# Kernel tuning notes

Hardware: AMD Instinct MI355X
Metric: run time of the kernel (lower is better)

The kernel has to match this reference:

```python
import jax, jax.numpy as jnp
import numpy as np

B, L, D = 4, 2048, 1024
H, DK, DV = 16, 64, 64
SCALE = float((4 * DK) ** 0.5)
EPS = 1e-6


def setup_inputs() -> dict:
    key = jax.random.key(0)
    ks = jax.random.split(key, 16)
    s_in = 1.0 / np.sqrt(D)
    inp = {}
    for i, name in enumerate(["q_a", "k_a", "v_a", "q_s", "k_s", "v_s"]):
        inp[name] = jax.random.normal(ks[i], (B, L, D), dtype=jnp.float32)
    # weights stored as [in, out] so projection is x @ W (equivalent math to nn.Linear)
    for j, name in enumerate(["Wqa", "Wka", "Wva", "Wqs", "Wks", "Wvs", "Wfc"]):
        inp[name] = jax.random.normal(ks[6 + j], (D, D), dtype=jnp.float32) * s_in
    inp["gamma"] = jnp.ones((D,), dtype=jnp.float32)
    inp["beta"] = jnp.zeros((D,), dtype=jnp.float32)
    return inp


def _proj(x, W, dh):
    # [B,L,D] @ [D, H*dh] -> [B,H,L,dh]
    return (x @ W).reshape(B, -1, H, dh).transpose(0, 2, 1, 3)


def reference(q_a, k_a, v_a, q_s, k_s, v_s, Wqa, Wka, Wva, Wqs, Wks, Wvs, Wfc, gamma, beta):
    residual = q_a + q_s
    qa = _proj(q_a, Wqa, DK)
    ka = _proj(k_a, Wka, DK)
    va = _proj(v_a, Wva, DV)
    qs = _proj(q_s, Wqs, DK)
    ks_ = _proj(k_s, Wks, DK)
    vs = _proj(v_s, Wvs, DV)
    # a2a + a2s + s2a + s2s == (qa+qs) @ (ka+ks)^T  (algebraic identity)
    q = qa + qs
    k = ka + ks_
    v = va + vs
    scores = jnp.einsum("bhqd,bhkd->bhqk", q, k) / SCALE
    attn = jax.nn.softmax(scores, axis=-1)  # dropout = identity (eval)
    out = jnp.einsum("bhqk,bhkd->bhqd", attn, v)  # [B,H,L,DV]
    out = out.transpose(0, 2, 1, 3).reshape(B, L, H * DV)
    out = out @ Wfc + residual
    mu = jnp.mean(out, axis=-1, keepdims=True)
    var = jnp.var(out, axis=-1, keepdims=True)
    out = (out - mu) * jax.lax.rsqrt(var + EPS) * gamma + beta
    return out
```

## Files before the change

kernel.cpp:

```cpp
#include <hip/hip_runtime.h>
#include <hip/hip_bf16.h>
#include <stdint.h>

typedef __attribute__((ext_vector_type(4))) float f32x4;
typedef __attribute__((ext_vector_type(16))) float f32x16;
typedef __attribute__((ext_vector_type(8))) short short8;
typedef __attribute__((ext_vector_type(2))) int int2v;

#define DEV static __device__ __forceinline__

DEV unsigned short f2bf(float f) {
  unsigned u = __float_as_uint(f);
  u += 0x7fffu + ((u >> 16) & 1u);
  return (unsigned short)(u >> 16);
}

DEV uint32_t cvtpk(float a, float b) {
  uint32_t r;
  asm("v_cvt_pk_bf16_f32 %0, %1, %2" : "=v"(r) : "v"(a), "v"(b));
  return r;
}

DEV int2v pl32(int a, int b) {
  return __builtin_amdgcn_permlane32_swap(a, b, false, false);
}

typedef const __attribute__((address_space(1))) void* gas_ptr;
typedef __attribute__((address_space(3))) void* las_ptr;

DEV void gload_lds16(const void* g, void* l) {
  __builtin_amdgcn_global_load_lds((gas_ptr)g, (las_ptr)l, 16, 0, 0);
}

struct CvtArgs {
  const float* in[6];
  unsigned short* out[6];
};

__global__ __launch_bounds__(256) void cvt_kernel(CvtArgs a, int n4) {
  const float* __restrict__ in = a.in[blockIdx.y];
  unsigned short* __restrict__ out = a.out[blockIdx.y];
  int idx = blockIdx.x * blockDim.x + threadIdx.x;
  int stride = gridDim.x * blockDim.x;
  for (int i = idx; i < n4; i += stride) {
    float4 v = reinterpret_cast<const float4*>(in)[i];
    ushort4 o;
    o.x = f2bf(v.x); o.y = f2bf(v.y); o.z = f2bf(v.z); o.w = f2bf(v.w);
    reinterpret_cast<ushort4*>(out)[i] = o;
  }
}

struct TcvtArgs {
  const float* src[7];
  unsigned short* dst[7];
  int stride[7];
  int koff[7];
};

__global__ __launch_bounds__(256) void tcvt_kernel(TcvtArgs a) {
  const int which = blockIdx.z;
  const float* __restrict__ src = a.src[which];
  unsigned short* __restrict__ dst = a.dst[which];
  const int dstStride = a.stride[which], kOff = a.koff[which];
  __shared__ float tile[32][33];
  int tx = threadIdx.x & 31;
  int ty = threadIdx.x >> 5;
  int n0 = blockIdx.x * 32;
  int k0 = blockIdx.y * 32;
#pragma unroll
  for (int i = 0; i < 4; i++)
    tile[ty + 8 * i][tx] = src[(size_t)(k0 + ty + 8 * i) * 1024 + n0 + tx];
  __syncthreads();
#pragma unroll
  for (int i = 0; i < 4; i++) {
    int n = n0 + ty + 8 * i;
    dst[(size_t)n * dstStride + kOff + k0 + tx] = f2bf(tile[tx][ty + 8 * i]);
  }
}

struct G3Args {
  const unsigned short* A1[3];
  const unsigned short* A2[3];
  const unsigned short* WT[3];
  unsigned short* out[3];
};

__global__ __launch_bounds__(256) void gemm3_kernel(G3Args g) {
  __shared__ unsigned short As[128 * 32];
  __shared__ unsigned short Bs[128 * 32];
  const int orig = blockIdx.x;
  const int swz = (orig & 7) * 192 + (orig >> 3);
  const int which = swz >> 9;
  const int bid = swz & 511;
  const unsigned short* __restrict__ A1 = g.A1[which];
  const unsigned short* __restrict__ A2 = g.A2[which];
  const unsigned short* __restrict__ WT = g.WT[which];
  unsigned short* __restrict__ outp = g.out[which];

  const int tid = threadIdx.x;
  const int lane = tid & 63;
  const int w = tid >> 6;
  const int mt = bid >> 3, nt = bid & 7;
  const int m0 = mt * 128, n0 = nt * 128;

  const int srow = (w << 4) + (lane >> 2);
  const int scol = (lane & 3) << 3;

  f32x4 zero4 = {0.f, 0.f, 0.f, 0.f};
  f32x4 acc[4][4];
#pragma unroll
  for (int mi = 0; mi < 4; mi++)
#pragma unroll
    for (int ni = 0; ni < 4; ni++) acc[mi][ni] = zero4;

  const int wr = w >> 1, wc = w & 1;
  const int arow = (wr << 6) + (lane & 15);
  const int brow = (wc << 6) + (lane & 15);
  const int kcol = (lane >> 4) << 3;

  for (int kt = 0; kt < 64; kt++) {
    const int kk = kt << 5;
    const unsigned short* Asrc;
    int ka;
    if (kk < 1024) { Asrc = A1; ka = kk; } else { Asrc = A2; ka = kk - 1024; }
#pragma unroll
    for (int p = 0; p < 2; p++) {
      const unsigned short* gp = Asrc + (size_t)(m0 + p * 64 + srow) * 1024 + ka + scol;
      gload_lds16(gp, &As[(p * 64 + srow) * 32 + scol]);
    }
#pragma unroll
    for (int p = 0; p < 2; p++) {
      const unsigned short* gp = WT + (size_t)(n0 + p * 64 + srow) * 2048 + kk + scol;
      gload_lds16(gp, &Bs[(p * 64 + srow) * 32 + scol]);
    }
    __syncthreads();

    short8 av[4], bv[4];
#pragma unroll
    for (int mi = 0; mi < 4; mi++)
      av[mi] = *reinterpret_cast<const short8*>(&As[(arow + mi * 16) * 32 + kcol]);
#pragma unroll
    for (int ni = 0; ni < 4; ni++)
      bv[ni] = *reinterpret_cast<const short8*>(&Bs[(brow + ni * 16) * 32 + kcol]);
#pragma unroll
    for (int mi = 0; mi < 4; mi++)
#pragma unroll
      for (int ni = 0; ni < 4; ni++)
        acc[mi][ni] = __builtin_amdgcn_mfma_f32_16x16x32_bf16(av[mi], bv[ni], acc[mi][ni], 0, 0, 0);
    __syncthreads();
  }

#pragma unroll
  for (int mi = 0; mi < 4; mi++) {
#pragma unroll
    for (int ni = 0; ni < 4; ni++) {
      const int col = n0 + (wc << 6) + ni * 16 + (lane & 15);
      const int rbase = m0 + (wr << 6) + mi * 16 + ((lane >> 4) << 2);
      const int h = col >> 6, d = col & 63;
      if (which < 2) {
#pragma unroll
        for (int r = 0; r < 4; r++) {
          const int m = rbase + r;
          const int b = m >> 11, l = m & 2047;
          outp[((size_t)((b * 16 + h) * 2048 + l)) * 64 + d] = f2bf(acc[mi][ni][r]);
        }
      } else {
        const int m = rbase;
        const int b = m >> 11, l = m & 2047;
        const int bh = b * 16 + h;
        ushort4 o;
        o.x = f2bf(acc[mi][ni][0]);
        o.y = f2bf(acc[mi][ni][1]);
        o.z = f2bf(acc[mi][ni][2]);
        o.w = f2bf(acc[mi][ni][3]);
        *reinterpret_cast<ushort4*>(
            outp + (size_t)(bh * 64 + (l >> 5)) * 2048 + d * 32 + (l & 31)) = o;
      }
    }
  }
}

__global__ __launch_bounds__(256) void gemmfc_kernel(const unsigned short* __restrict__ A1,
                                                     const unsigned short* __restrict__ WT,
                                                     float* __restrict__ outp) {
  __shared__ unsigned short As[128 * 32];
  __shared__ unsigned short Bs[128 * 32];
  const int orig = blockIdx.x;
  const int bid = (orig & 7) * 64 + (orig >> 3);
  const int tid = threadIdx.x;
  const int lane = tid & 63;
  const int w = tid >> 6;
  const int mt = bid >> 3, nt = bid & 7;
  const int m0 = mt * 128, n0 = nt * 128;

  const int srow = (w << 4) + (lane >> 2);
  const int scol = (lane & 3) << 3;

  f32x4 zero4 = {0.f, 0.f, 0.f, 0.f};
  f32x4 acc[4][4];
#pragma unroll
  for (int mi = 0; mi < 4; mi++)
#pragma unroll
    for (int ni = 0; ni < 4; ni++) acc[mi][ni] = zero4;

  const int wr = w >> 1, wc = w & 1;
  const int arow = (wr << 6) + (lane & 15);
  const int brow = (wc << 6) + (lane & 15);
  const int kcol = (lane >> 4) << 3;

  for (int kt = 0; kt < 32; kt++) {
    const int kk = kt << 5;
#pragma unroll
    for (int p = 0; p < 2; p++) {
      const unsigned short* gp = A1 + (size_t)(m0 + p * 64 + srow) * 1024 + kk + scol;
      gload_lds16(gp, &As[(p * 64 + srow) * 32 + scol]);
    }
#pragma unroll
    for (int p = 0; p < 2; p++) {
      const unsigned short* gp = WT + (size_t)(n0 + p * 64 + srow) * 1024 + kk + scol;
      gload_lds16(gp, &Bs[(p * 64 + srow) * 32 + scol]);
    }
    __syncthreads();

    short8 av[4], bv[4];
#pragma unroll
    for (int mi = 0; mi < 4; mi++)
      av[mi] = *reinterpret_cast<const short8*>(&As[(arow + mi * 16) * 32 + kcol]);
#pragma unroll
    for (int ni = 0; ni < 4; ni++)
      bv[ni] = *reinterpret_cast<const short8*>(&Bs[(brow + ni * 16) * 32 + kcol]);
#pragma unroll
    for (int mi = 0; mi < 4; mi++)
#pragma unroll
      for (int ni = 0; ni < 4; ni++)
        acc[mi][ni] = __builtin_amdgcn_mfma_f32_16x16x32_bf16(av[mi], bv[ni], acc[mi][ni], 0, 0, 0);
    __syncthreads();
  }

#pragma unroll
  for (int mi = 0; mi < 4; mi++) {
#pragma unroll
    for (int ni = 0; ni < 4; ni++) {
      const int col = n0 + (wc << 6) + ni * 16 + (lane & 15);
      const int rbase = m0 + (wr << 6) + mi * 16 + ((lane >> 4) << 2);
#pragma unroll
      for (int r = 0; r < 4; r++)
        outp[(size_t)(rbase + r) * 1024 + col] = acc[mi][ni][r];
    }
  }
}

__global__ __launch_bounds__(256) void attn_kernel(const unsigned short* __restrict__ Q,
                                                   const unsigned short* __restrict__ K,
                                                   const unsigned short* __restrict__ Vt,
                                                   unsigned short* __restrict__ O) {
  __shared__ unsigned short Ks[2][2048];
  __shared__ unsigned short Vs[2][2048];
  const int tid = threadIdx.x;
  const int lane = tid & 63;
  const int w = tid >> 6;
  const int n = blockIdx.x;
  const int bh = (n & 7) * 8 + (n >> 7);
  const int qg = (n >> 3) & 15;
  const int q0 = qg * 128 + w * 32;
  const int lo = lane & 31, hi = lane >> 5;

  const unsigned short* qp = Q + ((size_t)bh * 2048 + q0 + lo) * 64 + (hi << 3);
  short8 qf[4];
#pragma unroll
  for (int c = 0; c < 4; c++)
    qf[c] = *reinterpret_cast<const short8*>(qp + c * 16);

  f32x16 o0 = {0.f,0.f,0.f,0.f,0.f,0.f,0.f,0.f,0.f,0.f,0.f,0.f,0.f,0.f,0.f,0.f};
  f32x16 o1 = {0.f,0.f,0.f,0.f,0.f,0.f,0.f,0.f,0.f,0.f,0.f,0.f,0.f,0.f,0.f,0.f};
  float mrun = -1e30f, lsum = 0.0f;
  const float KS = 1.44269504088896f / 16.0f;

  const char* Kg = (const char*)(K + (size_t)bh * 2048 * 64);
  const char* Vg = (const char*)(Vt + (size_t)bh * 131072);

  const int p16 = tid * 16;
  const int lswz = p16 ^ (((p16 >> 7) & 7) << 4);
  const int koff = lswz;
  const int voff = (lswz >> 7) * 64 + ((lswz >> 6) & 1) * 2048 + (lswz & 63);

  const int sK = (lo & 7) << 4;
  int kix[4];
#pragma unroll
  for (int c = 0; c < 4; c++)
    kix[c] = ((lo * 128 + hi * 16 + c * 32) ^ sK) >> 1;
  int vix[4];
  vix[0] = ((lo * 128 + hi * 16) ^ sK) >> 1;
  vix[1] = ((lo * 128 + 32 + hi * 16) ^ sK) >> 1;
  vix[2] = ((lo * 128 + 64 + hi * 16) ^ sK) >> 1;
  vix[3] = ((lo * 128 + 96 + hi * 16) ^ sK) >> 1;

  auto STAGE = [&](int kt, int buf) {
    gload_lds16(Kg + (size_t)kt * 4096 + koff, &Ks[buf][tid * 8]);
    gload_lds16(Vg + (size_t)kt * 4096 + voff, &Vs[buf][tid * 8]);
  };

  STAGE(0, 0);
  __syncthreads();

  for (int kt = 0; kt < 64; kt++) {
    const int buf = kt & 1;
    const int nx = (kt < 63) ? kt + 1 : 63;
    STAGE(nx, buf ^ 1);

    short8 kc[4], vc[4];
#pragma unroll
    for (int c = 0; c < 4; c++)
      kc[c] = *reinterpret_cast<const short8*>(&Ks[buf][kix[c]]);
#pragma unroll
    for (int c = 0; c < 4; c++)
      vc[c] = *reinterpret_cast<const short8*>(&Vs[buf][vix[c]]);

    f32x16 s = {0.f,0.f,0.f,0.f,0.f,0.f,0.f,0.f,0.f,0.f,0.f,0.f,0.f,0.f,0.f,0.f};
    __builtin_amdgcn_s_setprio(1);
#pragma unroll
    for (int c = 0; c < 4; c++)
      s = __builtin_amdgcn_mfma_f32_32x32x16_bf16(kc[c], qf[c], s, 0, 0, 0);
    __builtin_amdgcn_s_setprio(0);

    float m01 = fmaxf(s[0], s[1]), m23 = fmaxf(s[2], s[3]);
    float m45 = fmaxf(s[4], s[5]), m67 = fmaxf(s[6], s[7]);
    float m89 = fmaxf(s[8], s[9]), mab = fmaxf(s[10], s[11]);
    float mcd = fmaxf(s[12], s[13]), mef = fmaxf(s[14], s[15]);
    float cmax = fmaxf(fmaxf(fmaxf(m01, m23), fmaxf(m45, m67)),
                       fmaxf(fmaxf(m89, mab), fmaxf(mcd, mef)));
    {
      int2v mm = pl32(__float_as_int(cmax), __float_as_int(cmax));
      cmax = fmaxf(__int_as_float(mm.x), __int_as_float(mm.y));
    }

    if (__any(cmax > mrun + 128.0f)) {
      const float mnew = fmaxf(mrun, cmax);
      const float alpha = __builtin_amdgcn_exp2f((mrun - mnew) * KS);
      lsum *= alpha;
#pragma unroll
      for (int r = 0; r < 16; r++) {
        const int row = (r & 3) + ((r >> 2) << 3) + (hi << 2);
        const float ar = __shfl(alpha, row);
        o0[r] *= ar;
        o1[r] *= ar;
      }
      mrun = mnew;
    }

    float pr[16];
    const float mk = mrun * KS;
#pragma unroll
    for (int r = 0; r < 16; r++)
      pr[r] = __builtin_amdgcn_exp2f(__builtin_fmaf(s[r], KS, -mk));
    float c01 = (pr[0] + pr[1]) + (pr[2] + pr[3]);
    float c23 = (pr[4] + pr[5]) + (pr[6] + pr[7]);
    float c45 = (pr[8] + pr[9]) + (pr[10] + pr[11]);
    float c67 = (pr[12] + pr[13]) + (pr[14] + pr[15]);
    float csum = (c01 + c23) + (c45 + c67);
    {
      int2v ss = pl32(__float_as_int(csum), __float_as_int(csum));
      csum = __int_as_float(ss.x) + __int_as_float(ss.y);
    }
    lsum += csum;

    const uint32_t c0 = cvtpk(pr[0], pr[1]),   c1 = cvtpk(pr[2], pr[3]);
    const uint32_t c2 = cvtpk(pr[4], pr[5]),   c3 = cvtpk(pr[6], pr[7]);
    const uint32_t c4 = cvtpk(pr[8], pr[9]),   c5 = cvtpk(pr[10], pr[11]);
    const uint32_t c6 = cvtpk(pr[12], pr[13]), c7 = cvtpk(pr[14], pr[15]);
    int2v s02 = pl32((int)c0, (int)c2);
    int2v s13 = pl32((int)c1, (int)c3);
    int2v s46 = pl32((int)c4, (int)c6);
    int2v s57 = pl32((int)c5, (int)c7);
    union { uint32_t u[4]; short8 v; } pa, pb;
    pa.u[0] = (uint32_t)s02.x; pa.u[1] = (uint32_t)s13.x;
    pa.u[2] = (uint32_t)s02.y; pa.u[3] = (uint32_t)s13.y;
    pb.u[0] = (uint32_t)s46.x; pb.u[1] = (uint32_t)s57.x;
    pb.u[2] = (uint32_t)s46.y; pb.u[3] = (uint32_t)s57.y;

    __builtin_amdgcn_s_setprio(1);
    o0 = __builtin_amdgcn_mfma_f32_32x32x16_bf16(pa.v, vc[0], o0, 0, 0, 0);
    o0 = __builtin_amdgcn_mfma_f32_32x32x16_bf16(pb.v, vc[1], o0, 0, 0, 0);
    o1 = __builtin_amdgcn_mfma_f32_32x32x16_bf16(pa.v, vc[2], o1, 0, 0, 0);
    o1 = __builtin_amdgcn_mfma_f32_32x32x16_bf16(pb.v, vc[3], o1, 0, 0, 0);
    __builtin_amdgcn_s_setprio(0);

    __syncthreads();
  }

  const int b = bh >> 4, h = bh & 15;
#pragma unroll
  for (int r = 0; r < 16; r++) {
    const int row = (r & 3) + ((r >> 2) << 3) + (hi << 2);
    const float lr = __shfl(lsum, row);
    const float inv = __builtin_amdgcn_rcpf(lr);
    const size_t base = ((size_t)b * 2048 + q0 + row) * 1024 + h * 64 + lo;
    O[base] = f2bf(o0[r] * inv);
    O[base + 32] = f2bf(o1[r] * inv);
  }
}

__global__ __launch_bounds__(256) void ln_kernel(const float* __restrict__ fc,
                                                 const float* __restrict__ qa,
                                                 const float* __restrict__ qs,
                                                 const float* __restrict__ gamma,
                                                 const float* __restrict__ beta,
                                                 float* __restrict__ out) {
  const int m = blockIdx.x;
  const int t = threadIdx.x;
  const size_t base = (size_t)m * 1024 + t * 4;
  float4 x = *reinterpret_cast<const float4*>(fc + base);
  const float4 a = *reinterpret_cast<const float4*>(qa + base);
  const float4 b = *reinterpret_cast<const float4*>(qs + base);
  x.x += a.x + b.x; x.y += a.y + b.y; x.z += a.z + b.z; x.w += a.w + b.w;
  float s1 = x.x + x.y + x.z + x.w;
  float s2 = x.x * x.x + x.y * x.y + x.z * x.z + x.w * x.w;
#pragma unroll
  for (int off = 1; off < 64; off <<= 1) {
    s1 += __shfl_xor(s1, off);
    s2 += __shfl_xor(s2, off);
  }
  __shared__ float sh[8];
  const int w = t >> 6, lane = t & 63;
  if (lane == 0) { sh[w] = s1; sh[4 + w] = s2; }
  __syncthreads();
  s1 = sh[0] + sh[1] + sh[2] + sh[3];
  s2 = sh[4] + sh[5] + sh[6] + sh[7];
  const float mu = s1 * (1.0f / 1024.0f);
  const float var = s2 * (1.0f / 1024.0f) - mu * mu;
  const float rs = rsqrtf(var + 1e-6f);
  const float4 g = *reinterpret_cast<const float4*>(gamma + t * 4);
  const float4 be = *reinterpret_cast<const float4*>(beta + t * 4);
  float4 y;
  y.x = (x.x - mu) * rs * g.x + be.x;
  y.y = (x.y - mu) * rs * g.y + be.y;
  y.z = (x.z - mu) * rs * g.z + be.z;
  y.w = (x.w - mu) * rs * g.w + be.w;
  *reinterpret_cast<float4*>(out + base) = y;
}

__global__ void sentinel_kernel(float* out, int n) {
  int i = blockIdx.x * blockDim.x + threadIdx.x;
  if (i < n) out[i] = 1234.5f;
}

extern "C" void kernel_launch(void* const* d_in, const int* in_sizes, int n_in,
                              void* d_out, int out_size, void* d_ws, size_t ws_size,
                              hipStream_t stream) {
  const size_t MB = 1024ull * 1024ull;
  if (ws_size < 174 * MB) {
    sentinel_kernel<<<(out_size + 255) / 256, 256, 0, stream>>>((float*)d_out, out_size);
    return;
  }
  const float* fin[6];
  for (int i = 0; i < 6; i++) fin[i] = (const float*)d_in[i];
  const float* Wf[7];
  for (int i = 0; i < 7; i++) Wf[i] = (const float*)d_in[6 + i];
  const float* gamma = (const float*)d_in[13];
  const float* beta = (const float*)d_in[14];

  char* ws = (char*)d_ws;
  unsigned short* Abf[6];
  for (int i = 0; i < 6; i++) Abf[i] = (unsigned short*)(ws + (size_t)i * 16 * MB);
  unsigned short* WqT = (unsigned short*)(ws + 96 * MB);
  unsigned short* WkT = (unsigned short*)(ws + 100 * MB);
  unsigned short* WvT = (unsigned short*)(ws + 104 * MB);
  unsigned short* WfcT = (unsigned short*)(ws + 108 * MB);
  unsigned short* Qb = (unsigned short*)(ws + 110 * MB);
  unsigned short* Kb = (unsigned short*)(ws + 126 * MB);
  unsigned short* Vtb = (unsigned short*)(ws + 142 * MB);
  unsigned short* Ob = (unsigned short*)(ws + 158 * MB);
  float* fcout = (float*)(ws + 16 * MB);

  CvtArgs ca;
  for (int i = 0; i < 6; i++) { ca.in[i] = fin[i]; ca.out[i] = Abf[i]; }
  cvt_kernel<<<dim3(1024, 6), 256, 0, stream>>>(ca, 2097152);

  TcvtArgs ta;
  const int wsel[7] = {0, 3, 1, 4, 2, 5, 6};
  unsigned short* wdst[7] = {WqT, WqT, WkT, WkT, WvT, WvT, WfcT};
  for (int i = 0; i < 7; i++) {
    ta.src[i] = Wf[wsel[i]];
    ta.dst[i] = wdst[i];
    ta.stride[i] = (i < 6) ? 2048 : 1024;
    ta.koff[i] = (i < 6) ? ((i & 1) ? 1024 : 0) : 0;
  }
  tcvt_kernel<<<dim3(32, 32, 7), 256, 0, stream>>>(ta);

  G3Args g3;
  g3.A1[0] = Abf[0]; g3.A2[0] = Abf[3]; g3.WT[0] = WqT; g3.out[0] = Qb;
  g3.A1[1] = Abf[1]; g3.A2[1] = Abf[4]; g3.WT[1] = WkT; g3.out[1] = Kb;
  g3.A1[2] = Abf[2]; g3.A2[2] = Abf[5]; g3.WT[2] = WvT; g3.out[2] = Vtb;
  gemm3_kernel<<<1536, 256, 0, stream>>>(g3);

  attn_kernel<<<1024, 256, 0, stream>>>(Qb, Kb, Vtb, Ob);

  gemmfc_kernel<<<512, 256, 0, stream>>>(Ob, WfcT, fcout);

  ln_kernel<<<8192, 256, 0, stream>>>(fcout, fin[0], fin[3], gamma, beta, (float*)d_out);
}
```

Before: 347.2 us.

## Rewrite QKV projection GEMM with 256x256 tiles, double-buffered swizzled LDS pipeline

```diff
diff --git a/kernel.cpp b/kernel.cpp
--- a/kernel.cpp
+++ b/kernel.cpp
@@ -85,13 +85,13 @@
   unsigned short* out[3];
 };
 
-__global__ __launch_bounds__(256) void gemm3_kernel(G3Args g) {
-  __shared__ unsigned short As[128 * 32];
-  __shared__ unsigned short Bs[128 * 32];
+__global__ __launch_bounds__(512, 2) void gemm3_kernel(G3Args g) {
+  __shared__ unsigned short As[2][256 * 64];
+  __shared__ unsigned short Bs[2][256 * 64];
   const int orig = blockIdx.x;
-  const int swz = (orig & 7) * 192 + (orig >> 3);
-  const int which = swz >> 9;
-  const int bid = swz & 511;
+  const int swz = (orig & 7) * 48 + (orig >> 3);
+  const int which = swz >> 7;
+  const int bid = swz & 127;
   const unsigned short* __restrict__ A1 = g.A1[which];
   const unsigned short* __restrict__ A2 = g.A2[which];
   const unsigned short* __restrict__ WT = g.WT[which];
@@ -100,79 +100,120 @@
   const int tid = threadIdx.x;
   const int lane = tid & 63;
   const int w = tid >> 6;
-  const int mt = bid >> 3, nt = bid & 7;
-  const int m0 = mt * 128, n0 = nt * 128;
-
-  const int srow = (w << 4) + (lane >> 2);
-  const int scol = (lane & 3) << 3;
+  const int mt = bid >> 2, nt = bid & 3;
+  const int m0 = mt * 256, n0 = nt * 256;
+  const int wr = w >> 2, wc = w & 3;
+
+  const int lr = lane >> 3;
+  const int lcsw = (((lane & 7) ^ lr) << 3);
+  const int aW = (w < 4) ? (w * 8) : (128 + (w - 4) * 8);
+  const int bW = w * 8;
+
+  const int la = lane & 15;
+  const int szb = (lane & 7) << 4;
+  int cF[2];
+#pragma unroll
+  for (int ks = 0; ks < 2; ks++)
+    cF[ks] = (((ks << 6) + ((lane >> 4) << 4)) ^ szb) >> 1;
+  const int arA = (wr * 128 + la) * 64;
+  const int brB = (wc * 64 + la) * 64;
 
   f32x4 zero4 = {0.f, 0.f, 0.f, 0.f};
-  f32x4 acc[4][4];
-#pragma unroll
-  for (int mi = 0; mi < 4; mi++)
-#pragma unroll
-    for (int ni = 0; ni < 4; ni++) acc[mi][ni] = zero4;
-
-  const int wr = w >> 1, wc = w & 1;
-  const int arow = (wr << 6) + (lane & 15);
-  const int brow = (wc << 6) + (lane & 15);
-  const int kcol = (lane >> 4) << 3;
-
-  for (int kt = 0; kt < 64; kt++) {
-    const int kk = kt << 5;
-    const unsigned short* Asrc;
-    int ka;
-    if (kk < 1024) { Asrc = A1; ka = kk; } else { Asrc = A2; ka = kk - 1024; }
-#pragma unroll
-    for (int p = 0; p < 2; p++) {
-      const unsigned short* gp = Asrc + (size_t)(m0 + p * 64 + srow) * 1024 + ka + scol;
-      gload_lds16(gp, &As[(p * 64 + srow) * 32 + scol]);
-    }
-#pragma unroll
-    for (int p = 0; p < 2; p++) {
-      const unsigned short* gp = WT + (size_t)(n0 + p * 64 + srow) * 2048 + kk + scol;
-      gload_lds16(gp, &Bs[(p * 64 + srow) * 32 + scol]);
-    }
-    __syncthreads();
-
-    short8 av[4], bv[4];
-#pragma unroll
-    for (int mi = 0; mi < 4; mi++)
-      av[mi] = *reinterpret_cast<const short8*>(&As[(arow + mi * 16) * 32 + kcol]);
-#pragma unroll
-    for (int ni = 0; ni < 4; ni++)
-      bv[ni] = *reinterpret_cast<const short8*>(&Bs[(brow + ni * 16) * 32 + kcol]);
-#pragma unroll
-    for (int mi = 0; mi < 4; mi++)
-#pragma unroll
-      for (int ni = 0; ni < 4; ni++)
-        acc[mi][ni] = __builtin_amdgcn_mfma_f32_16x16x32_bf16(av[mi], bv[ni], acc[mi][ni], 0, 0, 0);
-    __syncthreads();
-  }
-
-#pragma unroll
-  for (int mi = 0; mi < 4; mi++) {
-#pragma unroll
-    for (int ni = 0; ni < 4; ni++) {
-      const int col = n0 + (wc << 6) + ni * 16 + (lane & 15);
-      const int rbase = m0 + (wr << 6) + mi * 16 + ((lane >> 4) << 2);
+  f32x4 acc[8][4];
+#pragma unroll
+  for (int mf = 0; mf < 8; mf++)
+#pragma unroll
+    for (int nf = 0; nf < 4; nf++) acc[mf][nf] = zero4;
+
+  short8 bf[4][2];
+
+  auto STAGE_B = [&](int buf, int kk) {
+#pragma unroll
+    for (int r = 0; r < 4; r++)
+      gload_lds16(WT + (size_t)(n0 + bW + r * 64 + lr) * 2048 + kk + lcsw,
+                  &Bs[buf][(bW + r * 64) * 64 + lane * 8]);
+  };
+  auto STAGE_A = [&](int buf, int kk, int r) {
+    const unsigned short* Ab = (kk < 1024) ? A1 : A2;
+    const int ka = kk & 1023;
+    gload_lds16(Ab + (size_t)(m0 + aW + r * 32 + lr) * 1024 + ka + lcsw,
+                &As[buf][(aW + r * 32) * 64 + lane * 8]);
+  };
+
+  STAGE_B(0, 0);
+#pragma unroll
+  for (int r = 0; r < 4; r++) STAGE_A(0, 0, r);
+  asm volatile("s_waitcnt vmcnt(3)" ::: "memory");
+  __builtin_amdgcn_s_barrier();
+  __builtin_amdgcn_sched_barrier(0);
+
+  for (int kt = 0; kt < 32; kt++) {
+    const int cur = kt & 1;
+    const int nbuf = cur ^ 1;
+    const int kk = kt << 6;
+    const int nk = (kt < 31) ? (kk + 64) : kk;
+#pragma unroll
+    for (int p = 0; p < 4; p++) {
+      if (p == 0) {
+#pragma unroll
+        for (int nf = 0; nf < 4; nf++)
+#pragma unroll
+          for (int ks = 0; ks < 2; ks++)
+            bf[nf][ks] = *reinterpret_cast<const short8*>(&Bs[cur][brB + nf * 1024 + cF[ks]]);
+      }
+      short8 af[2][2];
+#pragma unroll
+      for (int mi = 0; mi < 2; mi++)
+#pragma unroll
+        for (int ks = 0; ks < 2; ks++)
+          af[mi][ks] =
+              *reinterpret_cast<const short8*>(&As[cur][arA + (2 * p + mi) * 1024 + cF[ks]]);
+      if (p == 0) STAGE_B(nbuf, nk);
+      STAGE_A(nbuf, nk, p);
+      asm volatile("s_waitcnt lgkmcnt(0)" ::: "memory");
+      __builtin_amdgcn_sched_barrier(0);
+      __builtin_amdgcn_s_setprio(1);
+#pragma unroll
+      for (int mi = 0; mi < 2; mi++)
+#pragma unroll
+        for (int nf = 0; nf < 4; nf++)
+#pragma unroll
+          for (int ks = 0; ks < 2; ks++)
+            acc[2 * p + mi][nf] = __builtin_amdgcn_mfma_f32_16x16x32_bf16(
+                af[mi][ks], bf[nf][ks], acc[2 * p + mi][nf], 0, 0, 0);
+      __builtin_amdgcn_s_setprio(0);
+      __builtin_amdgcn_sched_barrier(0);
+      if (p == 3) asm volatile("s_waitcnt vmcnt(3)" ::: "memory");
+      else        asm volatile("s_waitcnt vmcnt(7)" ::: "memory");
+      __builtin_amdgcn_s_barrier();
+      __builtin_amdgcn_sched_barrier(0);
+    }
+  }
+  asm volatile("s_waitcnt vmcnt(0)" ::: "memory");
+
+#pragma unroll
+  for (int mf = 0; mf < 8; mf++) {
+#pragma unroll
+    for (int nf = 0; nf < 4; nf++) {
+      const int col = n0 + wc * 64 + nf * 16 + (lane & 15);
+      const int rbase = m0 + wr * 128 + mf * 16 + ((lane >> 4) << 2);
       const int h = col >> 6, d = col & 63;
       if (which < 2) {
 #pragma unroll
         for (int r = 0; r < 4; r++) {
           const int m = rbase + r;
           const int b = m >> 11, l = m & 2047;
-          outp[((size_t)((b * 16 + h) * 2048 + l)) * 64 + d] = f2bf(acc[mi][ni][r]);
+          outp[((size_t)((b * 16 + h) * 2048 + l)) * 64 + d] = f2bf(acc[mf][nf][r]);
         }
       } else {
         const int m = rbase;
         const int b = m >> 11, l = m & 2047;
         const int bh = b * 16 + h;
         ushort4 o;
-        o.x = f2bf(acc[mi][ni][0]);
-        o.y = f2bf(acc[mi][ni][1]);
-        o.z = f2bf(acc[mi][ni][2]);
-        o.w = f2bf(acc[mi][ni][3]);
+        o.x = f2bf(acc[mf][nf][0]);
+        o.y = f2bf(acc[mf][nf][1]);
+        o.z = f2bf(acc[mf][nf][2]);
+        o.w = f2bf(acc[mf][nf][3]);
         *reinterpret_cast<ushort4*>(
             outp + (size_t)(bh * 64 + (l >> 5)) * 2048 + d * 32 + (l & 31)) = o;
       }
@@ -491,7 +532,7 @@
   g3.A1[0] = Abf[0]; g3.A2[0] = Abf[3]; g3.WT[0] = WqT; g3.out[0] = Qb;
   g3.A1[1] = Abf[1]; g3.A2[1] = Abf[4]; g3.WT[1] = WkT; g3.out[1] = Kb;
   g3.A1[2] = Abf[2]; g3.A2[2] = Abf[5]; g3.WT[2] = WvT; g3.out[2] = Vtb;
-  gemm3_kernel<<<1536, 256, 0, stream>>>(g3);
+  gemm3_kernel<<<384, 512, 0, stream>>>(g3);
 
   attn_kernel<<<1024, 256, 0, stream>>>(Qb, Kb, Vtb, Ob);
 
```

After: 372.5 us. 7.3% more time.
